# Kernel optimization log

Hardware: AMD Instinct MI355X
Metric: run time of the kernel (lower is better)

The kernel has to match this reference:

```python
import jax, jax.numpy as jnp
import numpy as np

TERNARY_THRESHOLD = 0.001

def _ternarize(t):
    # {-1, 0, 1} with dead zone of width 2*TERNARY_THRESHOLD
    return jnp.where(t > TERNARY_THRESHOLD, 1.0,
                     jnp.where(t < -TERNARY_THRESHOLD, -1.0, 0.0)).astype(t.dtype)

def setup_inputs() -> dict:
    key = jax.random.key(0)
    k_x, k_w1, k_b1, k_w2, k_b2 = jax.random.split(key, 5)
    B, D_IN, D_H, D_OUT = 65536, 784, 320, 10
    x = jax.random.normal(k_x, (B, D_IN), dtype=jnp.float32)
    # nn.Linear layout: weight [out_features, in_features]
    w1 = jax.random.normal(k_w1, (D_H, D_IN), dtype=jnp.float32) * 0.05
    b1 = jax.random.normal(k_b1, (D_H,), dtype=jnp.float32) * 0.05
    w2 = jax.random.normal(k_w2, (D_OUT, D_H), dtype=jnp.float32) * 0.05
    b2 = jax.random.normal(k_b2, (D_OUT,), dtype=jnp.float32) * 0.05
    return {"x": x, "w1": w1, "b1": b1, "w2": w2, "b2": b2}

def reference(x, w1, b1, w2, b2):
    x = x.reshape(-1, 784)
    # TernaryLinear: clamp weight to [-1,1], ternarize, then F.linear
    q1 = _ternarize(jnp.clip(w1, -1.0, 1.0))
    h = x @ q1.T + b1                       # [B, 320]
    h = _ternarize(h)                       # ternary activation
    q2 = _ternarize(jnp.clip(w2, -1.0, 1.0))
    logits = h @ q2.T + b2                  # [B, 10]
    return jax.nn.log_softmax(logits, axis=1)
```

## Files before the change

kernel.cpp:

```cpp
#include <hip/hip_runtime.h>
#include <stdint.h>


#define TERN_TH 0.001f

using bf16x8 = __attribute__((ext_vector_type(8))) short;
using f32x4  = __attribute__((ext_vector_type(4))) float;

__device__ __forceinline__ unsigned short f2bf(float f) {
    unsigned u = __float_as_uint(f);
    u = (u + 0x7FFFu + ((u >> 16) & 1u)) >> 16;
    return (unsigned short)u;
}
__device__ __forceinline__ float bf2f(unsigned short h) {
    return __uint_as_float(((unsigned)h) << 16);
}
__device__ __forceinline__ float ternf(float w) {
    return (w > TERN_TH) ? 1.0f : ((w < -TERN_TH) ? -1.0f : 0.0f);
}

#define Q1T_ELEMS (25 * 320 * 40)
__global__ void prep_q1(const float* __restrict__ w1, unsigned short* __restrict__ q1t) {
    int idx = blockIdx.x * 256 + threadIdx.x;
    if (idx >= Q1T_ELEMS) return;
    int c  = idx / (320 * 40);
    int r  = idx % (320 * 40);
    int j  = r / 40;
    int kk = r % 40;
    int k  = c * 32 + kk;
    float v = 0.0f;
    if (kk < 32 && k < 784) v = ternf(w1[j * 784 + k]);
    q1t[idx] = f2bf(v);
}

#define LDS_AHI 0
#define LDS_ALO 10240
#define LDS_B   20480
#define LDS_H   0
#define LDS_Q2  46080
#define LDS_TOTAL 56576

__global__ __launch_bounds__(256, 2) void mlp_main(
    const float* __restrict__ x, const unsigned short* __restrict__ q1t,
    const float* __restrict__ b1, const float* __restrict__ w2,
    const float* __restrict__ b2, float* __restrict__ out) {

    __shared__ __attribute__((aligned(16))) unsigned char smem[LDS_TOTAL];
    unsigned short* sm16 = (unsigned short*)smem;

    const int tid  = threadIdx.x;
    const int lane = tid & 63;
    const int wave = tid >> 6;
    const int quad = lane >> 4;
    const int l15  = lane & 15;
    const int wm   = wave >> 1;
    const int wn   = wave & 1;
    const int blk  = blockIdx.x;

    f32x4 acc[4][10];
#pragma unroll
    for (int mt = 0; mt < 4; ++mt)
#pragma unroll
        for (int nt = 0; nt < 10; ++nt) {
            f32x4 z = {0.f, 0.f, 0.f, 0.f};
            acc[mt][nt] = z;
        }

    const int srow  = tid >> 1;
    const int shalf = tid & 1;
    const float* xrow = x + (size_t)(blk * 128 + srow) * 784 + shalf * 16;

    for (int c = 0; c < 25; ++c) {
        __syncthreads();
        {
            float v[16];
            {
                float4 a0, a1, a2, a3;
                if (c < 24 || shalf == 0) {
                    const float4* s4 = (const float4*)(xrow + c * 32);
                    a0 = s4[0]; a1 = s4[1]; a2 = s4[2]; a3 = s4[3];
                } else {
                    a0.x = a0.y = a0.z = a0.w = 0.f;
                    a1 = a0; a2 = a0; a3 = a0;
                }
                v[0]=a0.x; v[1]=a0.y; v[2]=a0.z;  v[3]=a0.w;
                v[4]=a1.x; v[5]=a1.y; v[6]=a1.z;  v[7]=a1.w;
                v[8]=a2.x; v[9]=a2.y; v[10]=a2.z; v[11]=a2.w;
                v[12]=a3.x; v[13]=a3.y; v[14]=a3.z; v[15]=a3.w;
            }
            unsigned hw[8], lw[8];
#pragma unroll
            for (int i = 0; i < 8; ++i) {
                unsigned short h0 = f2bf(v[2 * i]);
                unsigned short h1 = f2bf(v[2 * i + 1]);
                unsigned short g0 = f2bf(v[2 * i]     - bf2f(h0));
                unsigned short g1 = f2bf(v[2 * i + 1] - bf2f(h1));
                hw[i] = (unsigned)h0 | ((unsigned)h1 << 16);
                lw[i] = (unsigned)g0 | ((unsigned)g1 << 16);
            }
            uint4* dh = (uint4*)(smem + LDS_AHI + srow * 80 + shalf * 32);
            dh[0] = make_uint4(hw[0], hw[1], hw[2], hw[3]);
            dh[1] = make_uint4(hw[4], hw[5], hw[6], hw[7]);
            uint4* dl = (uint4*)(smem + LDS_ALO + srow * 80 + shalf * 32);
            dl[0] = make_uint4(lw[0], lw[1], lw[2], lw[3]);
            dl[1] = make_uint4(lw[4], lw[5], lw[6], lw[7]);
        }
        {
            const uint4* src = (const uint4*)(q1t + c * 12800);
            uint4* dst = (uint4*)(smem + LDS_B);
#pragma unroll
            for (int i = 0; i < 7; ++i) {
                int idx = tid + i * 256;
                if (idx < 1600) dst[idx] = src[idx];
            }
        }
        __syncthreads();
        bf16x8 ahi[4], alo[4];
#pragma unroll
        for (int mt = 0; mt < 4; ++mt) {
            int row = wm * 64 + mt * 16 + l15;
            ahi[mt] = *(const bf16x8*)(smem + LDS_AHI + row * 80 + quad * 16);
            alo[mt] = *(const bf16x8*)(smem + LDS_ALO + row * 80 + quad * 16);
        }
#pragma unroll
        for (int nt = 0; nt < 10; ++nt) {
            int col = wn * 160 + nt * 16 + l15;
            bf16x8 bq = *(const bf16x8*)(smem + LDS_B + col * 80 + quad * 16);
#pragma unroll
            for (int mt = 0; mt < 4; ++mt) {
                acc[mt][nt] = __builtin_amdgcn_mfma_f32_16x16x32_bf16(ahi[mt], bq, acc[mt][nt], 0, 0, 0);
                acc[mt][nt] = __builtin_amdgcn_mfma_f32_16x16x32_bf16(alo[mt], bq, acc[mt][nt], 0, 0, 0);
            }
        }
    }

    __syncthreads();
    for (int idx = tid; idx < 16 * 328; idx += 256) {
        int o = idx / 328, j = idx % 328;
        float v = (o < 10 && j < 320) ? ternf(w2[o * 320 + j]) : 0.0f;
        sm16[(LDS_Q2 >> 1) + idx] = f2bf(v);
    }
    float b1v[10];
#pragma unroll
    for (int nt = 0; nt < 10; ++nt) b1v[nt] = b1[wn * 160 + nt * 16 + l15];
    float b2v = (l15 < 10) ? b2[l15] : 0.0f;

    for (int pass = 0; pass < 2; ++pass) {
        __syncthreads();
        if (wm == pass) {
#pragma unroll
            for (int mt = 0; mt < 4; ++mt)
#pragma unroll
                for (int nt = 0; nt < 10; ++nt)
#pragma unroll
                    for (int i = 0; i < 4; ++i) {
                        float hv = acc[mt][nt][i] + b1v[nt];
                        int row = mt * 16 + quad * 4 + i;
                        int col = wn * 160 + nt * 16 + l15;
                        sm16[(LDS_H >> 1) + row * 328 + col] = f2bf(ternf(hv));
                    }
        }
        __syncthreads();
        f32x4 acc2 = {0.f, 0.f, 0.f, 0.f};
#pragma unroll
        for (int kc = 0; kc < 10; ++kc) {
            bf16x8 a = *(const bf16x8*)(smem + LDS_H + (wave * 16 + l15) * 656 + kc * 64 + quad * 16);
            bf16x8 b = *(const bf16x8*)(smem + LDS_Q2 + l15 * 656 + kc * 64 + quad * 16);
            acc2 = __builtin_amdgcn_mfma_f32_16x16x32_bf16(a, b, acc2, 0, 0, 0);
        }
#pragma unroll
        for (int i = 0; i < 4; ++i) {
            float l  = acc2[i] + b2v;
            float lm = (l15 < 10) ? l : -3.4e38f;
#pragma unroll
            for (int s = 8; s >= 1; s >>= 1) lm = fmaxf(lm, __shfl_xor(lm, s, 64));
            float e  = (l15 < 10) ? expf(l - lm) : 0.0f;
            float ss = e;
#pragma unroll
            for (int s = 8; s >= 1; s >>= 1) ss += __shfl_xor(ss, s, 64);
            float ov = (l - lm) - logf(ss);
            if (l15 < 10) {
                int grow = blk * 128 + pass * 64 + wave * 16 + quad * 4 + i;
                out[(size_t)grow * 10 + l15] = ov;
            }
        }
    }
}

extern "C" void kernel_launch(void* const* d_in, const int* in_sizes, int n_in,
                              void* d_out, int out_size, void* d_ws, size_t ws_size,
                              hipStream_t stream) {
    const float* x  = (const float*)d_in[0];
    const float* w1 = (const float*)d_in[1];
    const float* b1 = (const float*)d_in[2];
    const float* w2 = (const float*)d_in[3];
    const float* b2 = (const float*)d_in[4];
    unsigned short* q1t = (unsigned short*)d_ws;

    prep_q1<<<(Q1T_ELEMS + 255) / 256, 256, 0, stream>>>(w1, q1t);
    mlp_main<<<512, 256, 0, stream>>>(x, q1t, b1, w2, b2, (float*)d_out);
}
```

Before: 342.3 us.

## Prefetch next x and weight chunks into registers to overlap with MFMA

Global loads for the next K-chunk of x and the ternary weight tile are issued into registers before the compute phase of the current chunk. The current chunk is written to LDS from registers, which hides global memory latency behind the MFMA work. The thread-to-row mapping also changes so that each half of the block loads one 16-float slice of a row. This adds about 44 live registers on top of a large accumulator array, which risks spills or reduced occupancy under launch_bounds(256,2).

After: 341.8 us. No clear change (-0.1%).

```diff
diff --git a/kernel.cpp b/kernel.cpp
--- a/kernel.cpp
+++ b/kernel.cpp
@@ -40,6 +40,8 @@
 #define LDS_Q2  46080
 #define LDS_TOTAL 56576
 
+#define BCHUNK_U4 1600
+
 __global__ __launch_bounds__(256, 2) void mlp_main(
     const float* __restrict__ x, const unsigned short* __restrict__ q1t,
     const float* __restrict__ b1, const float* __restrict__ w2,
@@ -66,28 +68,32 @@
             acc[mt][nt] = z;
         }
 
-    const int srow  = tid >> 1;
-    const int shalf = tid & 1;
+    const int srow  = tid & 127;
+    const int shalf = tid >> 7;
     const float* xrow = x + (size_t)(blk * 128 + srow) * 784 + shalf * 16;
+    const uint4* bsrc = (const uint4*)q1t;
+
+    float4 xr[4];
+    uint4  br[7];
+
+    {
+        const float4* s4 = (const float4*)(xrow);
+        xr[0] = s4[0]; xr[1] = s4[1]; xr[2] = s4[2]; xr[3] = s4[3];
+#pragma unroll
+        for (int i = 0; i < 7; ++i) {
+            int idx = tid + i * 256;
+            br[i] = (idx < BCHUNK_U4) ? bsrc[idx] : make_uint4(0, 0, 0, 0);
+        }
+    }
 
     for (int c = 0; c < 25; ++c) {
         __syncthreads();
         {
             float v[16];
-            {
-                float4 a0, a1, a2, a3;
-                if (c < 24 || shalf == 0) {
-                    const float4* s4 = (const float4*)(xrow + c * 32);
-                    a0 = s4[0]; a1 = s4[1]; a2 = s4[2]; a3 = s4[3];
-                } else {
-                    a0.x = a0.y = a0.z = a0.w = 0.f;
-                    a1 = a0; a2 = a0; a3 = a0;
-                }
-                v[0]=a0.x; v[1]=a0.y; v[2]=a0.z;  v[3]=a0.w;
-                v[4]=a1.x; v[5]=a1.y; v[6]=a1.z;  v[7]=a1.w;
-                v[8]=a2.x; v[9]=a2.y; v[10]=a2.z; v[11]=a2.w;
-                v[12]=a3.x; v[13]=a3.y; v[14]=a3.z; v[15]=a3.w;
-            }
+            v[0]=xr[0].x; v[1]=xr[0].y; v[2]=xr[0].z;  v[3]=xr[0].w;
+            v[4]=xr[1].x; v[5]=xr[1].y; v[6]=xr[1].z;  v[7]=xr[1].w;
+            v[8]=xr[2].x; v[9]=xr[2].y; v[10]=xr[2].z; v[11]=xr[2].w;
+            v[12]=xr[3].x; v[13]=xr[3].y; v[14]=xr[3].z; v[15]=xr[3].w;
             unsigned hw[8], lw[8];
 #pragma unroll
             for (int i = 0; i < 8; ++i) {
@@ -106,12 +112,27 @@
             dl[1] = make_uint4(lw[4], lw[5], lw[6], lw[7]);
         }
         {
-            const uint4* src = (const uint4*)(q1t + c * 12800);
             uint4* dst = (uint4*)(smem + LDS_B);
 #pragma unroll
             for (int i = 0; i < 7; ++i) {
                 int idx = tid + i * 256;
-                if (idx < 1600) dst[idx] = src[idx];
+                if (idx < BCHUNK_U4) dst[idx] = br[i];
+            }
+        }
+        if (c < 24) {
+            int cn = c + 1;
+            if (cn < 24 || shalf == 0) {
+                const float4* s4 = (const float4*)(xrow + cn * 32);
+                xr[0] = s4[0]; xr[1] = s4[1]; xr[2] = s4[2]; xr[3] = s4[3];
+            } else {
+                float4 z; z.x = z.y = z.z = z.w = 0.f;
+                xr[0] = z; xr[1] = z; xr[2] = z; xr[3] = z;
+            }
+            const uint4* src = bsrc + (size_t)cn * BCHUNK_U4;
+#pragma unroll
+            for (int i = 0; i < 7; ++i) {
+                int idx = tid + i * 256;
+                if (idx < BCHUNK_U4) br[i] = src[idx];
             }
         }
         __syncthreads();
```

## Load MFMA fragments directly from global memory, dropping LDS staging in main loop

Applied to the files above, without the earlier changes.

The ternarized W1 is pre-packed into MFMA fragment order so each lane reads its B operand straight from global memory (L2-resident). X rows are loaded and split into bf16 hi/lo directly in registers. This removes the LDS staging and both per-chunk barriers. Each wave now owns 32 rows by all 320 columns instead of a 64x160 tile. In exchange, B fragments are reread from cache by every wave rather than shared through LDS, the X loads per lane are less coalesced (32-byte pieces from 16 different rows), and the loop has no software prefetch to hide global latency.

Result: slower. 406.9 us (+18.9%).

```diff
diff --git a/kernel.cpp b/kernel.cpp
--- a/kernel.cpp
+++ b/kernel.cpp
@@ -19,29 +19,40 @@
     return (w > TERN_TH) ? 1.0f : ((w < -TERN_TH) ? -1.0f : 0.0f);
 }
 
-#define Q1T_ELEMS (25 * 320 * 40)
-__global__ void prep_q1(const float* __restrict__ w1, unsigned short* __restrict__ q1t) {
-    int idx = blockIdx.x * 256 + threadIdx.x;
-    if (idx >= Q1T_ELEMS) return;
-    int c  = idx / (320 * 40);
-    int r  = idx % (320 * 40);
-    int j  = r / 40;
-    int kk = r % 40;
-    int k  = c * 32 + kk;
-    float v = 0.0f;
-    if (kk < 32 && k < 784) v = ternf(w1[j * 784 + k]);
-    q1t[idx] = f2bf(v);
+__device__ __forceinline__ void split8(float4 a, float4 b, bf16x8& hi, bf16x8& lo) {
+    float v[8] = {a.x, a.y, a.z, a.w, b.x, b.y, b.z, b.w};
+    bf16x8 h, l;
+#pragma unroll
+    for (int i = 0; i < 8; ++i) {
+        unsigned short hh = f2bf(v[i]);
+        h[i] = (short)hh;
+        l[i] = (short)f2bf(v[i] - bf2f(hh));
+    }
+    hi = h; lo = l;
 }
 
-#define LDS_AHI 0
-#define LDS_ALO 10240
-#define LDS_B   20480
+#define Q1F_ELEMS (25 * 20 * 4 * 16 * 8)
+__global__ void prep_q1(const float* __restrict__ w1, unsigned short* __restrict__ q1f) {
+    int idx = blockIdx.x * 256 + threadIdx.x;
+    if (idx >= Q1F_ELEMS) return;
+    int kk   = idx & 7;
+    int col  = (idx >> 3) & 15;
+    int quad = (idx >> 7) & 3;
+    int t    = idx >> 9;
+    int nt   = t % 20;
+    int c    = t / 20;
+    int k = c * 32 + quad * 8 + kk;
+    int j = nt * 16 + col;
+    float v = (k < 784) ? ternf(w1[j * 784 + k]) : 0.0f;
+    q1f[idx] = f2bf(v);
+}
+
 #define LDS_H   0
-#define LDS_Q2  46080
-#define LDS_TOTAL 56576
+#define LDS_Q2  41984
+#define LDS_TOTAL 52480
 
 __global__ __launch_bounds__(256, 2) void mlp_main(
-    const float* __restrict__ x, const unsigned short* __restrict__ q1t,
+    const float* __restrict__ x, const unsigned short* __restrict__ q1f,
     const float* __restrict__ b1, const float* __restrict__ w2,
     const float* __restrict__ b2, float* __restrict__ out) {
 
@@ -53,110 +64,69 @@
     const int wave = tid >> 6;
     const int quad = lane >> 4;
     const int l15  = lane & 15;
-    const int wm   = wave >> 1;
-    const int wn   = wave & 1;
     const int blk  = blockIdx.x;
 
-    f32x4 acc[4][10];
+    f32x4 acc[2][20];
 #pragma unroll
-    for (int mt = 0; mt < 4; ++mt)
+    for (int mt = 0; mt < 2; ++mt)
 #pragma unroll
-        for (int nt = 0; nt < 10; ++nt) {
+        for (int nt = 0; nt < 20; ++nt) {
             f32x4 z = {0.f, 0.f, 0.f, 0.f};
             acc[mt][nt] = z;
         }
 
-    const int srow  = tid >> 1;
-    const int shalf = tid & 1;
-    const float* xrow = x + (size_t)(blk * 128 + srow) * 784 + shalf * 16;
+    const int rowbase = blk * 128 + wave * 32;
+    const float* xr0 = x + (size_t)(rowbase + l15) * 784;
+    const float* xr1 = x + (size_t)(rowbase + 16 + l15) * 784;
+    const unsigned short* bq1 = q1f + (size_t)quad * 128 + (size_t)l15 * 8;
 
     for (int c = 0; c < 25; ++c) {
-        __syncthreads();
+        int kq  = c * 32 + quad * 8;
+        int kqs = (kq < 784) ? kq : 0;
+
+        bf16x8 ahi0, alo0, ahi1, alo1;
         {
-            float v[16];
-            {
-                float4 a0, a1, a2, a3;
-                if (c < 24 || shalf == 0) {
-                    const float4* s4 = (const float4*)(xrow + c * 32);
-                    a0 = s4[0]; a1 = s4[1]; a2 = s4[2]; a3 = s4[3];
-                } else {
-                    a0.x = a0.y = a0.z = a0.w = 0.f;
-                    a1 = a0; a2 = a0; a3 = a0;
-                }
-                v[0]=a0.x; v[1]=a0.y; v[2]=a0.z;  v[3]=a0.w;
-                v[4]=a1.x; v[5]=a1.y; v[6]=a1.z;  v[7]=a1.w;
-                v[8]=a2.x; v[9]=a2.y; v[10]=a2.z; v[11]=a2.w;
-                v[12]=a3.x; v[13]=a3.y; v[14]=a3.z; v[15]=a3.w;
-            }
-            unsigned hw[8], lw[8];
+            const float4* p0 = (const float4*)(xr0 + kqs);
+            const float4* p1 = (const float4*)(xr1 + kqs);
+            float4 a0 = p0[0], b0 = p0[1];
+            float4 a1 = p1[0], b1_ = p1[1];
+            split8(a0, b0, ahi0, alo0);
+            split8(a1, b1_, ahi1, alo1);
+        }
+
+        const unsigned short* bp = bq1 + (size_t)c * 10240;
 #pragma unroll
-            for (int i = 0; i < 8; ++i) {
-                unsigned short h0 = f2bf(v[2 * i]);
-                unsigned short h1 = f2bf(v[2 * i + 1]);
-                unsigned short g0 = f2bf(v[2 * i]     - bf2f(h0));
-                unsigned short g1 = f2bf(v[2 * i + 1] - bf2f(h1));
-                hw[i] = (unsigned)h0 | ((unsigned)h1 << 16);
-                lw[i] = (unsigned)g0 | ((unsigned)g1 << 16);
-            }
-            uint4* dh = (uint4*)(smem + LDS_AHI + srow * 80 + shalf * 32);
-            dh[0] = make_uint4(hw[0], hw[1], hw[2], hw[3]);
-            dh[1] = make_uint4(hw[4], hw[5], hw[6], hw[7]);
-            uint4* dl = (uint4*)(smem + LDS_ALO + srow * 80 + shalf * 32);
-            dl[0] = make_uint4(lw[0], lw[1], lw[2], lw[3]);
-            dl[1] = make_uint4(lw[4], lw[5], lw[6], lw[7]);
-        }
-        {
-            const uint4* src = (const uint4*)(q1t + c * 12800);
-            uint4* dst = (uint4*)(smem + LDS_B);
-#pragma unroll
-            for (int i = 0; i < 7; ++i) {
-                int idx = tid + i * 256;
-                if (idx < 1600) dst[idx] = src[idx];
-            }
-        }
-        __syncthreads();
-        bf16x8 ahi[4], alo[4];
-#pragma unroll
-        for (int mt = 0; mt < 4; ++mt) {
-            int row = wm * 64 + mt * 16 + l15;
-            ahi[mt] = *(const bf16x8*)(smem + LDS_AHI + row * 80 + quad * 16);
-            alo[mt] = *(const bf16x8*)(smem + LDS_ALO + row * 80 + quad * 16);
-        }
-#pragma unroll
-        for (int nt = 0; nt < 10; ++nt) {
-            int col = wn * 160 + nt * 16 + l15;
-            bf16x8 bq = *(const bf16x8*)(smem + LDS_B + col * 80 + quad * 16);
-#pragma unroll
-            for (int mt = 0; mt < 4; ++mt) {
-                acc[mt][nt] = __builtin_amdgcn_mfma_f32_16x16x32_bf16(ahi[mt], bq, acc[mt][nt], 0, 0, 0);
-                acc[mt][nt] = __builtin_amdgcn_mfma_f32_16x16x32_bf16(alo[mt], bq, acc[mt][nt], 0, 0, 0);
-            }
+        for (int nt = 0; nt < 20; ++nt) {
+            bf16x8 bq = *(const bf16x8*)(bp + (size_t)nt * 512);
+            acc[0][nt] = __builtin_amdgcn_mfma_f32_16x16x32_bf16(ahi0, bq, acc[0][nt], 0, 0, 0);
+            acc[0][nt] = __builtin_amdgcn_mfma_f32_16x16x32_bf16(alo0, bq, acc[0][nt], 0, 0, 0);
+            acc[1][nt] = __builtin_amdgcn_mfma_f32_16x16x32_bf16(ahi1, bq, acc[1][nt], 0, 0, 0);
+            acc[1][nt] = __builtin_amdgcn_mfma_f32_16x16x32_bf16(alo1, bq, acc[1][nt], 0, 0, 0);
         }
     }
 
-    __syncthreads();
     for (int idx = tid; idx < 16 * 328; idx += 256) {
         int o = idx / 328, j = idx % 328;
         float v = (o < 10 && j < 320) ? ternf(w2[o * 320 + j]) : 0.0f;
         sm16[(LDS_Q2 >> 1) + idx] = f2bf(v);
     }
-    float b1v[10];
+    float b1v[20];
 #pragma unroll
-    for (int nt = 0; nt < 10; ++nt) b1v[nt] = b1[wn * 160 + nt * 16 + l15];
+    for (int nt = 0; nt < 20; ++nt) b1v[nt] = b1[nt * 16 + l15];
     float b2v = (l15 < 10) ? b2[l15] : 0.0f;
 
     for (int pass = 0; pass < 2; ++pass) {
         __syncthreads();
-        if (wm == pass) {
+        if ((wave >> 1) == pass) {
 #pragma unroll
-            for (int mt = 0; mt < 4; ++mt)
+            for (int mt = 0; mt < 2; ++mt)
 #pragma unroll
-                for (int nt = 0; nt < 10; ++nt)
+                for (int nt = 0; nt < 20; ++nt)
 #pragma unroll
                     for (int i = 0; i < 4; ++i) {
                         float hv = acc[mt][nt][i] + b1v[nt];
-                        int row = mt * 16 + quad * 4 + i;
-                        int col = wn * 160 + nt * 16 + l15;
+                        int row = (wave & 1) * 32 + mt * 16 + quad * 4 + i;
+                        int col = nt * 16 + l15;
                         sm16[(LDS_H >> 1) + row * 328 + col] = f2bf(ternf(hv));
                     }
         }
@@ -195,8 +165,8 @@
     const float* b1 = (const float*)d_in[2];
     const float* w2 = (const float*)d_in[3];
     const float* b2 = (const float*)d_in[4];
-    unsigned short* q1t = (unsigned short*)d_ws;
+    unsigned short* q1f = (unsigned short*)d_ws;
 
-    prep_q1<<<(Q1T_ELEMS + 255) / 256, 256, 0, stream>>>(w1, q1t);
-    mlp_main<<<512, 256, 0, stream>>>(x, q1t, b1, w2, b2, (float*)d_out);
+    prep_q1<<<(Q1F_ELEMS + 255) / 256, 256, 0, stream>>>(w1, q1f);
+    mlp_main<<<512, 256, 0, stream>>>(x, q1f, b1, w2, b2, (float*)d_out);
 }
```
